# Kernel optimization log

Hardware: AMD Instinct MI355X
Metric: run time of the kernel (lower is better)

The kernel has to match this reference:

```python
import jax, jax.numpy as jnp
import numpy as np

S, B, H = 2048, 32, 1024

def setup_inputs() -> dict:
    key = jax.random.key(0)
    k1, k2, k3 = jax.random.split(key, 3)
    hidden = jax.random.normal(k1, (1, B, H), dtype=jnp.float32)
    encoder_outputs = jax.random.normal(k2, (S, B, H), dtype=jnp.float32)
    W = jax.random.normal(k3, (H, H), dtype=jnp.float32) * (1.0 / np.sqrt(H))
    b = jnp.zeros((H,), dtype=jnp.float32)
    return {"hidden": hidden, "encoder_outputs": encoder_outputs, "W": W, "b": b}

def reference(hidden, encoder_outputs, W, b):
    # method == 'general': energy[b,i] = hidden[0,b] . (W @ enc[i,b] + bias)
    # proj: [S, B, H] = enc @ W^T + b  (nn.Linear convention: y = x W^T + b)
    proj = jnp.einsum('sbh,kh->sbk', encoder_outputs, W) + b
    # scores: [B, S]
    scores = jnp.einsum('bh,sbh->bs', hidden[0], proj)
    attn = jax.nn.softmax(scores, axis=1)
    return attn[:, None, :]  # [B, 1, S]
```

## Files before the change

### kernel.cpp

```cpp
#include <hip/hip_runtime.h>
#include <math.h>

#define H 1024
#define S 2048
#define B 32

__global__ void __launch_bounds__(512)
proj_hidden_kernel(const float* __restrict__ hidden,
                   const float* __restrict__ W,
                   float* __restrict__ v) {
    __shared__ float hs[2][H];
    __shared__ float part[32][2][64];
    const int hc = blockIdx.x & 15;
    const int bg = blockIdx.x >> 4;
    const int hq = threadIdx.x & 15;
    const int kg = threadIdx.x >> 4;

    for (int i = threadIdx.x; i < 2 * H; i += 512)
        hs[i >> 10][i & 1023] = hidden[(bg * 2 + (i >> 10)) * H + (i & 1023)];
    __syncthreads();

    const int h = hc * 64 + hq * 4;
    float4 a0 = {0.f, 0.f, 0.f, 0.f};
    float4 a1 = {0.f, 0.f, 0.f, 0.f};
#pragma unroll 4
    for (int kk = 0; kk < 32; ++kk) {
        const int k = kg + 32 * kk;
        const float h0 = hs[0][k];
        const float h1 = hs[1][k];
        const float4 w = *reinterpret_cast<const float4*>(W + (size_t)k * H + h);
        a0.x = fmaf(h0, w.x, a0.x); a0.y = fmaf(h0, w.y, a0.y);
        a0.z = fmaf(h0, w.z, a0.z); a0.w = fmaf(h0, w.w, a0.w);
        a1.x = fmaf(h1, w.x, a1.x); a1.y = fmaf(h1, w.y, a1.y);
        a1.z = fmaf(h1, w.z, a1.z); a1.w = fmaf(h1, w.w, a1.w);
    }
    *reinterpret_cast<float4*>(&part[kg][0][hq * 4]) = a0;
    *reinterpret_cast<float4*>(&part[kg][1][hq * 4]) = a1;
    __syncthreads();

    if (threadIdx.x < 128) {
        const int bb = threadIdx.x >> 6;
        const int c  = threadIdx.x & 63;
        float sum = 0.f;
#pragma unroll 8
        for (int g = 0; g < 32; ++g) sum += part[g][bb][c];
        v[(bg * 2 + bb) * H + hc * 64 + c] = sum;
    }
}

__global__ void __launch_bounds__(512)
scores_kernel(const float* __restrict__ enc,
              const float* __restrict__ v,
              float* __restrict__ scores) {
    const int s0 = blockIdx.x * 4;
    const int b  = threadIdx.x >> 4;
    const int k  = threadIdx.x & 15;

    const float4* e0 = reinterpret_cast<const float4*>(enc + ((size_t)(s0 + 0) * B + b) * H);
    const float4* e1 = reinterpret_cast<const float4*>(enc + ((size_t)(s0 + 1) * B + b) * H);
    const float4* e2 = reinterpret_cast<const float4*>(enc + ((size_t)(s0 + 2) * B + b) * H);
    const float4* e3 = reinterpret_cast<const float4*>(enc + ((size_t)(s0 + 3) * B + b) * H);
    const float4* vb = reinterpret_cast<const float4*>(v + (size_t)b * H);

    float a0 = 0.f, a1 = 0.f, a2 = 0.f, a3 = 0.f;
#pragma unroll 4
    for (int j = 0; j < 16; ++j) {
        const int f = k + 16 * j;
        const float4 w  = vb[f];
        const float4 x0 = e0[f];
        const float4 x1 = e1[f];
        const float4 x2 = e2[f];
        const float4 x3 = e3[f];
        a0 = fmaf(x0.x, w.x, fmaf(x0.y, w.y, fmaf(x0.z, w.z, fmaf(x0.w, w.w, a0))));
        a1 = fmaf(x1.x, w.x, fmaf(x1.y, w.y, fmaf(x1.z, w.z, fmaf(x1.w, w.w, a1))));
        a2 = fmaf(x2.x, w.x, fmaf(x2.y, w.y, fmaf(x2.z, w.z, fmaf(x2.w, w.w, a2))));
        a3 = fmaf(x3.x, w.x, fmaf(x3.y, w.y, fmaf(x3.z, w.z, fmaf(x3.w, w.w, a3))));
    }
#pragma unroll
    for (int off = 8; off > 0; off >>= 1) {
        a0 += __shfl_down(a0, off, 16);
        a1 += __shfl_down(a1, off, 16);
        a2 += __shfl_down(a2, off, 16);
        a3 += __shfl_down(a3, off, 16);
    }
    if (k == 0) {
        float4 r = {a0, a1, a2, a3};
        *reinterpret_cast<float4*>(scores + (size_t)b * S + s0) = r;
    }
}

__global__ void __launch_bounds__(256)
softmax_kernel(const float* __restrict__ scores,
               float* __restrict__ out) {
    const int b    = blockIdx.x;
    const int tid  = threadIdx.x;
    const int wave = tid >> 6;
    const int lane = tid & 63;

    __shared__ float wmax[4];
    __shared__ float wsum[4];

    float x[8];
    float m = -INFINITY;
#pragma unroll
    for (int i = 0; i < 8; ++i) {
        x[i] = scores[(size_t)b * S + tid + i * 256];
        m = fmaxf(m, x[i]);
    }
#pragma unroll
    for (int off = 32; off > 0; off >>= 1)
        m = fmaxf(m, __shfl_down(m, off, 64));
    if (lane == 0) wmax[wave] = m;
    __syncthreads();
    m = fmaxf(fmaxf(wmax[0], wmax[1]), fmaxf(wmax[2], wmax[3]));

    float sum = 0.f;
#pragma unroll
    for (int i = 0; i < 8; ++i) {
        x[i] = __expf(x[i] - m);
        sum += x[i];
    }
#pragma unroll
    for (int off = 32; off > 0; off >>= 1)
        sum += __shfl_down(sum, off, 64);
    if (lane == 0) wsum[wave] = sum;
    __syncthreads();
    sum = (wsum[0] + wsum[1]) + (wsum[2] + wsum[3]);

    const float inv = 1.0f / sum;
#pragma unroll
    for (int i = 0; i < 8; ++i) {
        out[(size_t)b * S + tid + i * 256] = x[i] * inv;
    }
}

extern "C" void kernel_launch(void* const* d_in, const int* in_sizes, int n_in,
                              void* d_out, int out_size, void* d_ws, size_t ws_size,
                              hipStream_t stream) {
    const float* hidden = (const float*)d_in[0];
    const float* enc    = (const float*)d_in[1];
    const float* W      = (const float*)d_in[2];

    float* v      = (float*)d_ws;
    float* scores = v + (size_t)B * H;
    float* out    = (float*)d_out;

    proj_hidden_kernel<<<256, 512, 0, stream>>>(hidden, W, v);
    scores_kernel<<<S / 4, 512, 0, stream>>>(enc, v, scores);
    softmax_kernel<<<B, 256, 0, stream>>>(scores, out);
}
```

Measured before the change: 55.18 us.

## Fuse projection, scores and softmax into one cooperative kernel with grid syncs

Merges the three kernels into a single cooperative launch of 256 blocks that separates the phases with grid-wide syncs. The scores phase now handles 8 sequence positions per block instead of 4, and softmax runs on 32 of the blocks with 512 threads. The aim is to remove two kernel launches and the gaps between them. In exchange it pays for two grid barriers and runs the encoder pass with only 256 blocks, which may lower memory parallelism for the main bandwidth-bound stream.

```diff
diff --git a/kernel.cpp b/kernel.cpp
--- a/kernel.cpp
+++ b/kernel.cpp
@@ -1,136 +1,149 @@
 #include <hip/hip_runtime.h>
+#include <hip/hip_cooperative_groups.h>
 #include <math.h>
 
 #define H 1024
 #define S 2048
 #define B 32
 
-__global__ void __launch_bounds__(512)
-proj_hidden_kernel(const float* __restrict__ hidden,
-                   const float* __restrict__ W,
-                   float* __restrict__ v) {
+namespace cg = cooperative_groups;
+
+__global__ void __launch_bounds__(512, 2)
+fused_attn_kernel(const float* __restrict__ hidden,
+                  const float* __restrict__ enc,
+                  const float* __restrict__ W,
+                  float* __restrict__ v,
+                  float* __restrict__ scores,
+                  float* __restrict__ out) {
+    cg::grid_group grid = cg::this_grid();
+
     __shared__ float hs[2][H];
     __shared__ float part[32][2][64];
-    const int hc = blockIdx.x & 15;
-    const int bg = blockIdx.x >> 4;
-    const int hq = threadIdx.x & 15;
-    const int kg = threadIdx.x >> 4;
+    __shared__ float wred[8];
 
-    for (int i = threadIdx.x; i < 2 * H; i += 512)
-        hs[i >> 10][i & 1023] = hidden[(bg * 2 + (i >> 10)) * H + (i & 1023)];
-    __syncthreads();
+    {
+        const int hc = blockIdx.x & 15;
+        const int bg = blockIdx.x >> 4;
+        const int hq = threadIdx.x & 15;
+        const int kg = threadIdx.x >> 4;
 
-    const int h = hc * 64 + hq * 4;
-    float4 a0 = {0.f, 0.f, 0.f, 0.f};
-    float4 a1 = {0.f, 0.f, 0.f, 0.f};
+        for (int i = threadIdx.x; i < 2 * H; i += 512)
+            hs[i >> 10][i & 1023] = hidden[(bg * 2 + (i >> 10)) * H + (i & 1023)];
+        __syncthreads();
+
+        const int h = hc * 64 + hq * 4;
+        float4 a0 = {0.f, 0.f, 0.f, 0.f};
+        float4 a1 = {0.f, 0.f, 0.f, 0.f};
 #pragma unroll 4
-    for (int kk = 0; kk < 32; ++kk) {
-        const int k = kg + 32 * kk;
-        const float h0 = hs[0][k];
-        const float h1 = hs[1][k];
-        const float4 w = *reinterpret_cast<const float4*>(W + (size_t)k * H + h);
-        a0.x = fmaf(h0, w.x, a0.x); a0.y = fmaf(h0, w.y, a0.y);
-        a0.z = fmaf(h0, w.z, a0.z); a0.w = fmaf(h0, w.w, a0.w);
-        a1.x = fmaf(h1, w.x, a1.x); a1.y = fmaf(h1, w.y, a1.y);
-        a1.z = fmaf(h1, w.z, a1.z); a1.w = fmaf(h1, w.w, a1.w);
+        for (int kk = 0; kk < 32; ++kk) {
+            const int k = kg + 32 * kk;
+            const float h0 = hs[0][k];
+            const float h1 = hs[1][k];
+            const float4 w = *reinterpret_cast<const float4*>(W + (size_t)k * H + h);
+            a0.x = fmaf(h0, w.x, a0.x); a0.y = fmaf(h0, w.y, a0.y);
+            a0.z = fmaf(h0, w.z, a0.z); a0.w = fmaf(h0, w.w, a0.w);
+            a1.x = fmaf(h1, w.x, a1.x); a1.y = fmaf(h1, w.y, a1.y);
+            a1.z = fmaf(h1, w.z, a1.z); a1.w = fmaf(h1, w.w, a1.w);
+        }
+        *reinterpret_cast<float4*>(&part[kg][0][hq * 4]) = a0;
+        *reinterpret_cast<float4*>(&part[kg][1][hq * 4]) = a1;
+        __syncthreads();
+
+        if (threadIdx.x < 128) {
+            const int bb = threadIdx.x >> 6;
+            const int c  = threadIdx.x & 63;
+            float sum = 0.f;
+#pragma unroll 8
+            for (int g = 0; g < 32; ++g) sum += part[g][bb][c];
+            v[(bg * 2 + bb) * H + hc * 64 + c] = sum;
+        }
     }
-    *reinterpret_cast<float4*>(&part[kg][0][hq * 4]) = a0;
-    *reinterpret_cast<float4*>(&part[kg][1][hq * 4]) = a1;
-    __syncthreads();
 
-    if (threadIdx.x < 128) {
-        const int bb = threadIdx.x >> 6;
-        const int c  = threadIdx.x & 63;
+    grid.sync();
+
+    {
+        const int s0 = blockIdx.x * 8;
+        const int b  = threadIdx.x >> 4;
+        const int k  = threadIdx.x & 15;
+        const float4* vb = reinterpret_cast<const float4*>(v + (size_t)b * H);
+
+        for (int i = 0; i < 8; i += 4) {
+            const float4* e0 = reinterpret_cast<const float4*>(enc + ((size_t)(s0 + i + 0) * B + b) * H);
+            const float4* e1 = reinterpret_cast<const float4*>(enc + ((size_t)(s0 + i + 1) * B + b) * H);
+            const float4* e2 = reinterpret_cast<const float4*>(enc + ((size_t)(s0 + i + 2) * B + b) * H);
+            const float4* e3 = reinterpret_cast<const float4*>(enc + ((size_t)(s0 + i + 3) * B + b) * H);
+
+            float a0 = 0.f, a1 = 0.f, a2 = 0.f, a3 = 0.f;
+#pragma unroll 4
+            for (int j = 0; j < 16; ++j) {
+                const int f = k + 16 * j;
+                const float4 w  = vb[f];
+                const float4 x0 = e0[f];
+                const float4 x1 = e1[f];
+                const float4 x2 = e2[f];
+                const float4 x3 = e3[f];
+                a0 = fmaf(x0.x, w.x, fmaf(x0.y, w.y, fmaf(x0.z, w.z, fmaf(x0.w, w.w, a0))));
+                a1 = fmaf(x1.x, w.x, fmaf(x1.y, w.y, fmaf(x1.z, w.z, fmaf(x1.w, w.w, a1))));
+                a2 = fmaf(x2.x, w.x, fmaf(x2.y, w.y, fmaf(x2.z, w.z, fmaf(x2.w, w.w, a2))));
+                a3 = fmaf(x3.x, w.x, fmaf(x3.y, w.y, fmaf(x3.z, w.z, fmaf(x3.w, w.w, a3))));
+            }
+#pragma unroll
+            for (int off = 8; off > 0; off >>= 1) {
+                a0 += __shfl_down(a0, off, 16);
+                a1 += __shfl_down(a1, off, 16);
+                a2 += __shfl_down(a2, off, 16);
+                a3 += __shfl_down(a3, off, 16);
+            }
+            if (k == 0) {
+                float4 r = {a0, a1, a2, a3};
+                *reinterpret_cast<float4*>(scores + (size_t)b * S + s0 + i) = r;
+            }
+        }
+    }
+
+    grid.sync();
+
+    if (blockIdx.x < B) {
+        const int b    = blockIdx.x;
+        const int tid  = threadIdx.x;
+        const int wave = tid >> 6;
+        const int lane = tid & 63;
+
+        float x[4];
+        float m = -INFINITY;
+#pragma unroll
+        for (int i = 0; i < 4; ++i) {
+            x[i] = scores[(size_t)b * S + tid + i * 512];
+            m = fmaxf(m, x[i]);
+        }
+#pragma unroll
+        for (int off = 32; off > 0; off >>= 1)
+            m = fmaxf(m, __shfl_down(m, off, 64));
+        if (lane == 0) wred[wave] = m;
+        __syncthreads();
+#pragma unroll
+        for (int w = 0; w < 8; ++w) m = fmaxf(m, wred[w]);
+        __syncthreads();
+
         float sum = 0.f;
-#pragma unroll 8
-        for (int g = 0; g < 32; ++g) sum += part[g][bb][c];
-        v[(bg * 2 + bb) * H + hc * 64 + c] = sum;
-    }
-}
+#pragma unroll
+        for (int i = 0; i < 4; ++i) {
+            x[i] = __expf(x[i] - m);
+            sum += x[i];
+        }
+#pragma unroll
+        for (int off = 32; off > 0; off >>= 1)
+            sum += __shfl_down(sum, off, 64);
+        if (lane == 0) wred[wave] = sum;
+        __syncthreads();
+        sum = 0.f;
+#pragma unroll
+        for (int w = 0; w < 8; ++w) sum += wred[w];
 
-__global__ void __launch_bounds__(512)
-scores_kernel(const float* __restrict__ enc,
-              const float* __restrict__ v,
-              float* __restrict__ scores) {
-    const int s0 = blockIdx.x * 4;
-    const int b  = threadIdx.x >> 4;
-    const int k  = threadIdx.x & 15;
-
-    const float4* e0 = reinterpret_cast<const float4*>(enc + ((size_t)(s0 + 0) * B + b) * H);
-    const float4* e1 = reinterpret_cast<const float4*>(enc + ((size_t)(s0 + 1) * B + b) * H);
-    const float4* e2 = reinterpret_cast<const float4*>(enc + ((size_t)(s0 + 2) * B + b) * H);
-    const float4* e3 = reinterpret_cast<const float4*>(enc + ((size_t)(s0 + 3) * B + b) * H);
-    const float4* vb = reinterpret_cast<const float4*>(v + (size_t)b * H);
-
-    float a0 = 0.f, a1 = 0.f, a2 = 0.f, a3 = 0.f;
-#pragma unroll 4
-    for (int j = 0; j < 16; ++j) {
-        const int f = k + 16 * j;
-        const float4 w  = vb[f];
-        const float4 x0 = e0[f];
-        const float4 x1 = e1[f];
-        const float4 x2 = e2[f];
-        const float4 x3 = e3[f];
-        a0 = fmaf(x0.x, w.x, fmaf(x0.y, w.y, fmaf(x0.z, w.z, fmaf(x0.w, w.w, a0))));
-        a1 = fmaf(x1.x, w.x, fmaf(x1.y, w.y, fmaf(x1.z, w.z, fmaf(x1.w, w.w, a1))));
-        a2 = fmaf(x2.x, w.x, fmaf(x2.y, w.y, fmaf(x2.z, w.z, fmaf(x2.w, w.w, a2))));
-        a3 = fmaf(x3.x, w.x, fmaf(x3.y, w.y, fmaf(x3.z, w.z, fmaf(x3.w, w.w, a3))));
-    }
+        const float inv = 1.0f / sum;
 #pragma unroll
-    for (int off = 8; off > 0; off >>= 1) {
-        a0 += __shfl_down(a0, off, 16);
-        a1 += __shfl_down(a1, off, 16);
-        a2 += __shfl_down(a2, off, 16);
-        a3 += __shfl_down(a3, off, 16);
-    }
-    if (k == 0) {
-        float4 r = {a0, a1, a2, a3};
-        *reinterpret_cast<float4*>(scores + (size_t)b * S + s0) = r;
-    }
-}
-
-__global__ void __launch_bounds__(256)
-softmax_kernel(const float* __restrict__ scores,
-               float* __restrict__ out) {
-    const int b    = blockIdx.x;
-    const int tid  = threadIdx.x;
-    const int wave = tid >> 6;
-    const int lane = tid & 63;
-
-    __shared__ float wmax[4];
-    __shared__ float wsum[4];
-
-    float x[8];
-    float m = -INFINITY;
-#pragma unroll
-    for (int i = 0; i < 8; ++i) {
-        x[i] = scores[(size_t)b * S + tid + i * 256];
-        m = fmaxf(m, x[i]);
-    }
-#pragma unroll
-    for (int off = 32; off > 0; off >>= 1)
-        m = fmaxf(m, __shfl_down(m, off, 64));
-    if (lane == 0) wmax[wave] = m;
-    __syncthreads();
-    m = fmaxf(fmaxf(wmax[0], wmax[1]), fmaxf(wmax[2], wmax[3]));
-
-    float sum = 0.f;
-#pragma unroll
-    for (int i = 0; i < 8; ++i) {
-        x[i] = __expf(x[i] - m);
-        sum += x[i];
-    }
-#pragma unroll
-    for (int off = 32; off > 0; off >>= 1)
-        sum += __shfl_down(sum, off, 64);
-    if (lane == 0) wsum[wave] = sum;
-    __syncthreads();
-    sum = (wsum[0] + wsum[1]) + (wsum[2] + wsum[3]);
-
-    const float inv = 1.0f / sum;
-#pragma unroll
-    for (int i = 0; i < 8; ++i) {
-        out[(size_t)b * S + tid + i * 256] = x[i] * inv;
+        for (int i = 0; i < 4; ++i)
+            out[(size_t)b * S + tid + i * 512] = x[i] * inv;
     }
 }
 
@@ -145,7 +158,8 @@
     float* scores = v + (size_t)B * H;
     float* out    = (float*)d_out;
 
-    proj_hidden_kernel<<<256, 512, 0, stream>>>(hidden, W, v);
-    scores_kernel<<<S / 4, 512, 0, stream>>>(enc, v, scores);
-    softmax_kernel<<<B, 256, 0, stream>>>(scores, out);
+    void* args[] = {(void*)&hidden, (void*)&enc, (void*)&W,
+                    (void*)&v, (void*)&scores, (void*)&out};
+    hipLaunchCooperativeKernel((const void*)fused_attn_kernel,
+                               dim3(256), dim3(512), args, 0, stream);
 }
```

Result: slower. 115.0 us (+108.4%).
